# Optimization experiments

Hardware: AMD Instinct MI355X
Metric: run time of the kernel (lower is better)

## Reference

```python
import jax, jax.numpy as jnp
import numpy as np

LN_EPS = 1e-5

def layer_norm(x, w, b):
    m = jnp.mean(x, axis=-1, keepdims=True)
    v = jnp.mean((x - m) ** 2, axis=-1, keepdims=True)
    return (x - m) * jax.lax.rsqrt(v + LN_EPS) * w + b

def setup_inputs() -> dict:
    key = jax.random.key(0)
    ks = jax.random.split(key, 10)
    B, N, L = 32, 576, 100
    low, high = 1024, 1536
    inp = {
        "vit_feat": jax.random.normal(ks[0], (B, N, low), dtype=jnp.float32),
        "box_feat": jax.random.normal(ks[1], (B, L, high), dtype=jnp.float32),
        "lengths": jax.random.randint(ks[2], (B,), 0, L, dtype=jnp.int64),
        # query projector: LayerNorm(low) + Linear(low, low)
        "q_ln_w": jnp.ones((low,), jnp.float32),
        "q_ln_b": jnp.zeros((low,), jnp.float32),
        "q_w": jax.random.normal(ks[3], (low, low), dtype=jnp.float32) * 0.02,
        "q_b": jnp.zeros((low,), jnp.float32),
        # key projector: LayerNorm(high) + Linear(high, low)
        "k_ln_w": jnp.ones((high,), jnp.float32),
        "k_ln_b": jnp.zeros((high,), jnp.float32),
        "k_w": jax.random.normal(ks[4], (high, low), dtype=jnp.float32) * 0.02,
        "k_b": jnp.zeros((low,), jnp.float32),
        # value projector: LayerNorm(high) + Linear(high, low)
        "v_ln_w": jnp.ones((high,), jnp.float32),
        "v_ln_b": jnp.zeros((high,), jnp.float32),
        "v_w": jax.random.normal(ks[5], (high, low), dtype=jnp.float32) * 0.02,
        "v_b": jnp.zeros((low,), jnp.float32),
    }
    return inp

def reference(vit_feat, box_feat, lengths,
              q_ln_w, q_ln_b, q_w, q_b,
              k_ln_w, k_ln_b, k_w, k_b,
              v_ln_w, v_ln_b, v_w, v_b):
    B, L = box_feat.shape[0], box_feat.shape[1]
    # padding mask, same as the original per-row copy loop
    mask = jnp.arange(L)[None, :] < lengths[:, None]          # [B, L] bool
    q = layer_norm(vit_feat, q_ln_w, q_ln_b) @ q_w + q_b      # [B, N, low]
    k = layer_norm(box_feat, k_ln_w, k_ln_b) @ k_w + k_b      # [B, L, low]
    v = layer_norm(box_feat, v_ln_w, v_ln_b) @ v_w + v_b      # [B, L, low]
    scale = 1.0 / jnp.sqrt(jnp.asarray(k.shape[-1], q.dtype))
    att = jnp.einsum('bnd,bld->bnl', q, k * scale)            # [B, N, L]
    att = jnp.where(mask[:, None, :], att, -jnp.inf)
    att = jnp.nan_to_num(att)  # -inf -> finite min, matching torch nan_to_num
    att = jax.nn.softmax(att, axis=-1)
    out = jnp.einsum('bnl,bld->bnd', att, v)                  # [B, N, low]
    return vit_feat + out
```

## Files before the change

kernel.cpp:

```cpp
#include <hip/hip_runtime.h>
#include <stdint.h>

typedef __attribute__((ext_vector_type(8))) short short8;
typedef __attribute__((ext_vector_type(4))) float f32x4;

#define NEG_FLT_MAX (-3.402823466e38f)

__device__ __forceinline__ unsigned short f2bf(float f) {
  uint32_t u = __float_as_uint(f);
  uint32_t r = (u + 0x7fffu + ((u >> 16) & 1u)) >> 16;
  return (unsigned short)r;
}

__device__ __forceinline__ float bf2f(unsigned short u) {
  return __uint_as_float(((uint32_t)u) << 16);
}

__device__ __forceinline__ void gload16(const void* g, void* l) {
  __builtin_amdgcn_global_load_lds(
      (const __attribute__((address_space(1))) uint32_t*)g,
      (__attribute__((address_space(3))) uint32_t*)l, 16, 0, 0);
}

__global__ void tpv_kernel(const float* __restrict__ src, unsigned short* __restrict__ dst) {
  __shared__ float tile[32][33];
  const int c0 = blockIdx.x * 32;
  const int r0 = blockIdx.y * 32;
  const int tx = threadIdx.x, ty = threadIdx.y;
#pragma unroll
  for (int i = ty; i < 32; i += 8)
    tile[i][tx] = src[(size_t)(r0 + i) * 1024 + (c0 + tx)];
  __syncthreads();
#pragma unroll
  for (int i = ty; i < 32; i += 8)
    dst[(size_t)(c0 + i) * 1536 + (r0 + tx)] = f2bf(tile[tx][i]);
}

__global__ __launch_bounds__(256) void wconv_kernel(
    const float* __restrict__ qw, const float* __restrict__ kw,
    unsigned short* __restrict__ qwb, unsigned short* __restrict__ kwb, float scale) {
  const int idx = blockIdx.x * 256 + threadIdx.x;
  const int QG = 1024 * 1024 / 4;
  if (idx < QG) {
    float4 v = ((const float4*)qw)[idx];
    ushort4 o;
    o.x = f2bf(v.x); o.y = f2bf(v.y); o.z = f2bf(v.z); o.w = f2bf(v.w);
    ((ushort4*)qwb)[idx] = o;
  } else {
    const int j = idx - QG;
    float4 v = ((const float4*)kw)[j];
    ushort4 o;
    o.x = f2bf(v.x * scale); o.y = f2bf(v.y * scale);
    o.z = f2bf(v.z * scale); o.w = f2bf(v.w * scale);
    ((ushort4*)kwb)[j] = o;
  }
}

__global__ __launch_bounds__(256) void wvec_kernel(
    const float* __restrict__ qw, const float* __restrict__ kw,
    const float* __restrict__ qb, const float* __restrict__ kb, float scale,
    float* __restrict__ bias3, float* __restrict__ w4, float* __restrict__ c4) {
  const int wv = threadIdx.x >> 6, l = threadIdx.x & 63;
  const int idx = blockIdx.x;
  float s = 0.f;
  if (idx < 256) {
    const int i = idx * 4 + wv;
    const float* row = qw + (size_t)i * 1024;
#pragma unroll
    for (int s0 = 0; s0 < 1024; s0 += 256) {
      float4 a = *(const float4*)(row + s0 + l * 4);
      float4 b = *(const float4*)(kb + s0 + l * 4);
      s += a.x * b.x + a.y * b.y + a.z * b.z + a.w * b.w;
    }
#pragma unroll
    for (int off = 32; off; off >>= 1) s += __shfl_xor(s, off);
    if (l == 0) bias3[i] = s * scale;
  } else if (idx < 640) {
    const int j = (idx - 256) * 4 + wv;
    const float* row = kw + (size_t)j * 1024;
#pragma unroll
    for (int s0 = 0; s0 < 1024; s0 += 256) {
      float4 a = *(const float4*)(row + s0 + l * 4);
      float4 b = *(const float4*)(qb + s0 + l * 4);
      s += a.x * b.x + a.y * b.y + a.z * b.z + a.w * b.w;
    }
#pragma unroll
    for (int off = 32; off; off >>= 1) s += __shfl_xor(s, off);
    if (l == 0) w4[j] = s * scale;
  } else if (wv == 0) {
#pragma unroll
    for (int s0 = 0; s0 < 1024; s0 += 256) {
      float4 a = *(const float4*)(qb + s0 + l * 4);
      float4 b = *(const float4*)(kb + s0 + l * 4);
      s += a.x * b.x + a.y * b.y + a.z * b.z + a.w * b.w;
    }
#pragma unroll
    for (int off = 32; off; off >>= 1) s += __shfl_xor(s, off);
    if (l == 0) *c4 = s * scale;
  }
}

__device__ __forceinline__ void block_reduce2(float& s, float& ss, float* red) {
#pragma unroll
  for (int off = 32; off > 0; off >>= 1) {
    s += __shfl_xor(s, off);
    ss += __shfl_xor(ss, off);
  }
  const int wave = threadIdx.x >> 6;
  const int lane = threadIdx.x & 63;
  if (lane == 0) { red[wave * 2] = s; red[wave * 2 + 1] = ss; }
  __syncthreads();
  if (threadIdx.x == 0) {
    float a = 0.f, b = 0.f;
    for (int i = 0; i < 4; i++) { a += red[i * 2]; b += red[i * 2 + 1]; }
    red[0] = a; red[1] = b;
  }
  __syncthreads();
  s = red[0]; ss = red[1];
}

__global__ __launch_bounds__(256) void ln_vit_kernel(
    const float* __restrict__ x, const float* __restrict__ w,
    const float* __restrict__ b, unsigned short* __restrict__ out) {
  __shared__ float red[8];
  const int row = blockIdx.x;
  const int t = threadIdx.x;
  const float4 v = ((const float4*)(x + (size_t)row * 1024))[t];
  float s = v.x + v.y + v.z + v.w;
  float ss = v.x * v.x + v.y * v.y + v.z * v.z + v.w * v.w;
  block_reduce2(s, ss, red);
  const float m = s * (1.f / 1024.f);
  const float var = ss * (1.f / 1024.f) - m * m;
  const float rstd = rsqrtf(var + 1e-5f);
  const float4 w4 = ((const float4*)w)[t];
  const float4 b4 = ((const float4*)b)[t];
  ushort4 o;
  o.x = f2bf((v.x - m) * rstd * w4.x + b4.x);
  o.y = f2bf((v.y - m) * rstd * w4.y + b4.y);
  o.z = f2bf((v.z - m) * rstd * w4.z + b4.z);
  o.w = f2bf((v.w - m) * rstd * w4.w + b4.w);
  ((ushort4*)(out + (size_t)row * 1024))[t] = o;
}

__global__ __launch_bounds__(256) void ln_box_kernel(
    const float* __restrict__ x,
    const float* __restrict__ kw, const float* __restrict__ kb,
    const float* __restrict__ vw, const float* __restrict__ vb,
    unsigned short* __restrict__ kn, unsigned short* __restrict__ vn) {
  __shared__ float red[8];
  const int row = blockIdx.x;
  const int t = threadIdx.x;
  const float4* xr = (const float4*)(x + (size_t)row * 1536);
  const float4 a = xr[t];
  float4 c = make_float4(0.f, 0.f, 0.f, 0.f);
  if (t < 128) c = xr[256 + t];
  float s = a.x + a.y + a.z + a.w + c.x + c.y + c.z + c.w;
  float ss = a.x * a.x + a.y * a.y + a.z * a.z + a.w * a.w +
             c.x * c.x + c.y * c.y + c.z * c.z + c.w * c.w;
  block_reduce2(s, ss, red);
  const float m = s * (1.f / 1536.f);
  const float var = ss * (1.f / 1536.f) - m * m;
  const float rstd = rsqrtf(var + 1e-5f);
  {
    const float4 w4 = ((const float4*)kw)[t];
    const float4 b4 = ((const float4*)kb)[t];
    ushort4 o;
    o.x = f2bf((a.x - m) * rstd * w4.x + b4.x);
    o.y = f2bf((a.y - m) * rstd * w4.y + b4.y);
    o.z = f2bf((a.z - m) * rstd * w4.z + b4.z);
    o.w = f2bf((a.w - m) * rstd * w4.w + b4.w);
    ((ushort4*)(kn + (size_t)row * 1536))[t] = o;
    const float4 w4v = ((const float4*)vw)[t];
    const float4 b4v = ((const float4*)vb)[t];
    o.x = f2bf((a.x - m) * rstd * w4v.x + b4v.x);
    o.y = f2bf((a.y - m) * rstd * w4v.y + b4v.y);
    o.z = f2bf((a.z - m) * rstd * w4v.z + b4v.z);
    o.w = f2bf((a.w - m) * rstd * w4v.w + b4v.w);
    ((ushort4*)(vn + (size_t)row * 1536))[t] = o;
  }
  if (t < 128) {
    const int t2 = 256 + t;
    const float4 w4 = ((const float4*)kw)[t2];
    const float4 b4 = ((const float4*)kb)[t2];
    ushort4 o;
    o.x = f2bf((c.x - m) * rstd * w4.x + b4.x);
    o.y = f2bf((c.y - m) * rstd * w4.y + b4.y);
    o.z = f2bf((c.z - m) * rstd * w4.z + b4.z);
    o.w = f2bf((c.w - m) * rstd * w4.w + b4.w);
    ((ushort4*)(kn + (size_t)row * 1536))[t2] = o;
    const float4 w4v = ((const float4*)vw)[t2];
    const float4 b4v = ((const float4*)vb)[t2];
    o.x = f2bf((c.x - m) * rstd * w4v.x + b4v.x);
    o.y = f2bf((c.y - m) * rstd * w4v.y + b4v.y);
    o.z = f2bf((c.z - m) * rstd * w4v.z + b4v.z);
    o.w = f2bf((c.w - m) * rstd * w4v.w + b4v.w);
    ((ushort4*)(vn + (size_t)row * 1536))[t2] = o;
  }
}

__global__ __launch_bounds__(256) void qbk_kernel(
    const unsigned short* __restrict__ kn, const float* __restrict__ w4,
    const float* __restrict__ c4, float* __restrict__ qbk) {
  const int wv = threadIdx.x >> 6, l = threadIdx.x & 63;
  const int row = blockIdx.x * 4 + wv;
  const unsigned short* r = kn + (size_t)row * 1536;
  float s = 0.f;
#pragma unroll
  for (int s0 = 0; s0 < 1536; s0 += 512) {
    short8 v = *(const short8*)(r + s0 + l * 8);
    const float* wp = w4 + s0 + l * 8;
    float4 w0 = *(const float4*)wp;
    float4 w1 = *(const float4*)(wp + 4);
    s += bf2f((unsigned short)v[0]) * w0.x + bf2f((unsigned short)v[1]) * w0.y +
         bf2f((unsigned short)v[2]) * w0.z + bf2f((unsigned short)v[3]) * w0.w +
         bf2f((unsigned short)v[4]) * w1.x + bf2f((unsigned short)v[5]) * w1.y +
         bf2f((unsigned short)v[6]) * w1.z + bf2f((unsigned short)v[7]) * w1.w;
  }
#pragma unroll
  for (int off = 32; off; off >>= 1) s += __shfl_xor(s, off);
  if (l == 0) qbk[row] = s + *c4;
}

__device__ __forceinline__ void gemm_core64(
    const unsigned short* __restrict__ A, int lda, int rowmaxA, int tm0,
    const unsigned short* __restrict__ Bt, int ldb, int rowmaxB, int tn0,
    int K, unsigned short* As, unsigned short* Bs, f32x4 acc[4][4]) {
  const int tid = threadIdx.x;
  const int w = tid >> 6, l = tid & 63;
  const int wr = w >> 1, wc = w & 1;
  const int srow = (w << 4) + (l >> 2);
  const int scol = (l & 3) << 3;
  int ra0 = tm0 + srow;      if (ra0 > rowmaxA) ra0 = rowmaxA;
  int ra1 = tm0 + srow + 64; if (ra1 > rowmaxA) ra1 = rowmaxA;
  int rb0 = tn0 + srow;      if (rb0 > rowmaxB) rb0 = rowmaxB;
  int rb1 = tn0 + srow + 64; if (rb1 > rowmaxB) rb1 = rowmaxB;
  const unsigned short* pa0 = A + (size_t)ra0 * lda + scol;
  const unsigned short* pa1 = A + (size_t)ra1 * lda + scol;
  const unsigned short* pb0 = Bt + (size_t)rb0 * ldb + scol;
  const unsigned short* pb1 = Bt + (size_t)rb1 * ldb + scol;
  unsigned short* la0 = As + (w << 4) * 32;
  unsigned short* la1 = As + ((w << 4) + 64) * 32;
  unsigned short* lb0 = Bs + (w << 4) * 32;
  unsigned short* lb1 = Bs + ((w << 4) + 64) * 32;
  const int foff = ((l & 15) << 5) + ((l >> 4) << 3);
  const unsigned short* fa = As + (wr << 6) * 32 + foff;
  const unsigned short* fb = Bs + (wc << 6) * 32 + foff;
#pragma unroll
  for (int i = 0; i < 4; i++)
#pragma unroll
    for (int j = 0; j < 4; j++) acc[i][j] = (f32x4)0.0f;
  for (int k0 = 0; k0 < K; k0 += 64) {
    gload16(pa0 + k0, la0);
    gload16(pa1 + k0, la1);
    gload16(pb0 + k0, lb0);
    gload16(pb1 + k0, lb1);
    gload16(pa0 + k0 + 32, la0 + 4096);
    gload16(pa1 + k0 + 32, la1 + 4096);
    gload16(pb0 + k0 + 32, lb0 + 4096);
    gload16(pb1 + k0 + 32, lb1 + 4096);
    __syncthreads();
    {
      short8 a[4], b[4];
#pragma unroll
      for (int i = 0; i < 4; i++) a[i] = *(const short8*)(fa + i * 512);
#pragma unroll
      for (int j = 0; j < 4; j++) b[j] = *(const short8*)(fb + j * 512);
#pragma unroll
      for (int i = 0; i < 4; i++)
#pragma unroll
        for (int j = 0; j < 4; j++)
          acc[i][j] = __builtin_amdgcn_mfma_f32_16x16x32_bf16(a[i], b[j], acc[i][j], 0, 0, 0);
    }
    {
      short8 a[4], b[4];
#pragma unroll
      for (int i = 0; i < 4; i++) a[i] = *(const short8*)(fa + 4096 + i * 512);
#pragma unroll
      for (int j = 0; j < 4; j++) b[j] = *(const short8*)(fb + 4096 + j * 512);
#pragma unroll
      for (int i = 0; i < 4; i++)
#pragma unroll
        for (int j = 0; j < 4; j++)
          acc[i][j] = __builtin_amdgcn_mfma_f32_16x16x32_bf16(a[i], b[j], acc[i][j], 0, 0, 0);
    }
    __syncthreads();
  }
}

__global__ __launch_bounds__(256) void gemm_w3_kernel(
    const unsigned short* __restrict__ qwb, const unsigned short* __restrict__ kwb,
    unsigned short* __restrict__ W3) {
  __shared__ unsigned short As[128 * 64];
  __shared__ unsigned short Bs[128 * 64];
  const int tm0 = blockIdx.x * 128, tn0 = blockIdx.y * 128;
  f32x4 acc[4][4];
  gemm_core64(qwb, 1024, 1023, tm0, kwb, 1024, 1535, tn0, 1024, As, Bs, acc);
  const int tid = threadIdx.x;
  const int w = tid >> 6, l = tid & 63;
  const int wr = w >> 1, wc = w & 1;
#pragma unroll
  for (int i = 0; i < 4; i++) {
    const int row0 = tm0 + wr * 64 + i * 16 + (l >> 4) * 4;
#pragma unroll
    for (int j = 0; j < 4; j++) {
      const int col = tn0 + wc * 64 + j * 16 + (l & 15);
#pragma unroll
      for (int r = 0; r < 4; r++)
        W3[(size_t)(row0 + r) * 1536 + col] = f2bf(acc[i][j][r]);
    }
  }
}

__global__ __launch_bounds__(256) void gemm_kv_kernel(
    const unsigned short* __restrict__ kn, const unsigned short* __restrict__ vn,
    const unsigned short* __restrict__ W3, const unsigned short* __restrict__ vwt,
    const float* __restrict__ bias3, const float* __restrict__ vb,
    unsigned short* __restrict__ kq, unsigned short* __restrict__ vT) {
  __shared__ unsigned short As[128 * 64];
  __shared__ unsigned short Bs[128 * 64];
  const int z = blockIdx.z;
  const unsigned short* A = z ? vn : kn;
  const unsigned short* Bt = z ? vwt : W3;
  const float* bias = z ? vb : bias3;
  const int M = 3200, N = 1024, K = 1536;
  const int tm0 = blockIdx.x * 128, tn0 = blockIdx.y * 128;
  f32x4 acc[4][4];
  gemm_core64(A, K, M - 1, tm0, Bt, K, N - 1, tn0, K, As, Bs, acc);
  const int tid = threadIdx.x;
  const int w = tid >> 6, l = tid & 63;
  const int wr = w >> 1, wc = w & 1;
#pragma unroll
  for (int i = 0; i < 4; i++) {
    const int row0 = tm0 + wr * 64 + i * 16 + (l >> 4) * 4;
#pragma unroll
    for (int j = 0; j < 4; j++) {
      const int col = tn0 + wc * 64 + j * 16 + (l & 15);
      const float bv = bias[col];
#pragma unroll
      for (int r = 0; r < 4; r++) {
        const int row = row0 + r;
        const float val = acc[i][j][r] + bv;
        if (!z) {
          kq[(size_t)row * N + col] = f2bf(val);
        } else {
          const int bb = row / 100;
          const int ll = row - bb * 100;
          vT[((size_t)bb * N + col) * 128 + ll] = f2bf(val);
        }
      }
    }
  }
}

__global__ __launch_bounds__(256) void attfused_kernel(
    const unsigned short* __restrict__ qn, const unsigned short* __restrict__ kq,
    const unsigned short* __restrict__ vT, const float* __restrict__ qbk,
    const int* __restrict__ lengths, const float* __restrict__ vit,
    float* __restrict__ out) {
  __shared__ __align__(16) char smem[53248];
  unsigned short* As = (unsigned short*)smem;
  unsigned short* Bs = (unsigned short*)(smem + 8192);
  float* Smat = (float*)smem;
  float* invr = (float*)(smem + 34816);
  float* qb_l = (float*)(smem + 35072);
  unsigned short* P = (unsigned short*)(smem + 36864);

  const int b = blockIdx.y;
  const int tm0 = blockIdx.x * 64;
  const int t = threadIdx.x;
  const int w = t >> 6, l = t & 63;
  if (t < 128) qb_l[t] = (t < 100) ? qbk[b * 100 + t] : 0.f;

  const unsigned short* A = qn + (size_t)b * 576 * 1024;
  const unsigned short* B = kq + (size_t)b * 100 * 1024;
  const int sr = t >> 2;
  const int sc8 = (t & 3) << 3;
  const unsigned short* pa = A + (size_t)(tm0 + sr) * 1024 + sc8;
  const unsigned short* pb0 = B + (size_t)sr * 1024 + sc8;
  int rb1 = 64 + sr; if (rb1 > 99) rb1 = 99;
  const unsigned short* pb1 = B + (size_t)rb1 * 1024 + sc8;
  unsigned short* la = As + (w << 9);
  unsigned short* lb0 = Bs + (w << 9);
  unsigned short* lb1 = Bs + 2048 + (w << 9);
  const int foff = ((l & 15) << 5) + ((l >> 4) << 3);
  const unsigned short* fa = As + foff;
  const unsigned short* fb = Bs + (w << 5) * 32 + foff;

  f32x4 acc[4][2];
#pragma unroll
  for (int i = 0; i < 4; i++) { acc[i][0] = (f32x4)0.0f; acc[i][1] = (f32x4)0.0f; }

  for (int k0 = 0; k0 < 1024; k0 += 64) {
    gload16(pa + k0, la);
    gload16(pb0 + k0, lb0);
    gload16(pb1 + k0, lb1);
    gload16(pa + k0 + 32, la + 2048);
    gload16(pb0 + k0 + 32, lb0 + 4096);
    gload16(pb1 + k0 + 32, lb1 + 4096);
    __syncthreads();
    {
      short8 a[4], bf[2];
#pragma unroll
      for (int i = 0; i < 4; i++) a[i] = *(const short8*)(fa + i * 512);
#pragma unroll
      for (int j = 0; j < 2; j++) bf[j] = *(const short8*)(fb + j * 512);
#pragma unroll
      for (int i = 0; i < 4; i++)
#pragma unroll
        for (int j = 0; j < 2; j++)
          acc[i][j] = __builtin_amdgcn_mfma_f32_16x16x32_bf16(a[i], bf[j], acc[i][j], 0, 0, 0);
    }
    {
      short8 a[4], bf[2];
#pragma unroll
      for (int i = 0; i < 4; i++) a[i] = *(const short8*)(fa + 2048 + i * 512);
#pragma unroll
      for (int j = 0; j < 2; j++) bf[j] = *(const short8*)(fb + 4096 + j * 512);
#pragma unroll
      for (int i = 0; i < 4; i++)
#pragma unroll
        for (int j = 0; j < 2; j++)
          acc[i][j] = __builtin_amdgcn_mfma_f32_16x16x32_bf16(a[i], bf[j], acc[i][j], 0, 0, 0);
    }
    __syncthreads();
  }

#pragma unroll
  for (int i = 0; i < 4; i++) {
    const int r0 = i * 16 + (l >> 4) * 4;
#pragma unroll
    for (int j = 0; j < 2; j++) {
      const int c = (w << 5) + j * 16 + (l & 15);
      const float qb = qb_l[c];
#pragma unroll
      for (int rr = 0; rr < 4; rr++) Smat[c * 68 + r0 + rr] = acc[i][j][rr] + qb;
    }
  }
  __syncthreads();

  const int r = t >> 2, g = t & 3;
  const int len = lengths[b];
  float mx = NEG_FLT_MAX;
#pragma unroll
  for (int i = 0; i < 25; i++) {
    const int ll = g * 25 + i;
    const float v = (ll < len) ? Smat[ll * 68 + r] : NEG_FLT_MAX;
    mx = fmaxf(mx, v);
  }
  mx = fmaxf(mx, __shfl_xor(mx, 1));
  mx = fmaxf(mx, __shfl_xor(mx, 2));
  float sum = 0.f;
#pragma unroll
  for (int i = 0; i < 25; i++) {
    const int ll = g * 25 + i;
    const float v = (ll < len) ? Smat[ll * 68 + r] : NEG_FLT_MAX;
    const float e = __expf(v - mx);
    Smat[ll * 68 + r] = e;
    sum += e;
  }
  sum += __shfl_xor(sum, 1);
  sum += __shfl_xor(sum, 2);
  if (g == 0) invr[r] = 1.f / sum;
  __syncthreads();

  {
    const float inv = invr[r];
    ushort4* prow = (ushort4*)(P + r * 128);
#pragma unroll
    for (int j = 0; j < 8; j++) {
      const int c0 = g * 32 + j * 4;
      ushort4 o;
      o.x = (c0 + 0 < 100) ? f2bf(Smat[(c0 + 0) * 68 + r] * inv) : (unsigned short)0;
      o.y = (c0 + 1 < 100) ? f2bf(Smat[(c0 + 1) * 68 + r] * inv) : (unsigned short)0;
      o.z = (c0 + 2 < 100) ? f2bf(Smat[(c0 + 2) * 68 + r] * inv) : (unsigned short)0;
      o.w = (c0 + 3 < 100) ? f2bf(Smat[(c0 + 3) * 68 + r] * inv) : (unsigned short)0;
      prow[g * 8 + j] = o;
    }
  }
  __syncthreads();

  const unsigned short* vTb = vT + (size_t)b * 131072;
  const float* vitb = vit + ((size_t)b * 576 + tm0) * 1024;
  float* outb = out + ((size_t)b * 576 + tm0) * 1024;
  for (int nt = 0; nt < 8; ++nt) {
    {
      const unsigned short* src = vTb + (size_t)nt * 16384 + ((t >> 4) * 128) + ((t & 15) * 8);
#pragma unroll
      for (int i = 0; i < 8; i++)
        gload16(src + i * 2048, smem + i * 4096 + w * 1024);
    }
    __syncthreads();
    f32x4 acc2[4][2];
#pragma unroll
    for (int i = 0; i < 4; i++) { acc2[i][0] = (f32x4)0.0f; acc2[i][1] = (f32x4)0.0f; }
#pragma unroll
    for (int ks = 0; ks < 4; ks++) {
      short8 av[4], bv[2];
#pragma unroll
      for (int i = 0; i < 4; i++)
        av[i] = *(const short8*)(smem + 36864 + (i * 16 + (l & 15)) * 256 + ks * 64 + ((l >> 4) << 4));
#pragma unroll
      for (int j = 0; j < 2; j++)
        bv[j] = *(const short8*)(smem + (w * 32 + j * 16 + (l & 15)) * 256 + ks * 64 + ((l >> 4) << 4));
#pragma unroll
      for (int i = 0; i < 4; i++)
#pragma unroll
        for (int j = 0; j < 2; j++)
          acc2[i][j] = __builtin_amdgcn_mfma_f32_16x16x32_bf16(av[i], bv[j], acc2[i][j], 0, 0, 0);
    }
    __syncthreads();
    {
      float* E = (float*)smem;
#pragma unroll
      for (int i = 0; i < 4; i++) {
        const int row0 = i * 16 + (l >> 4) * 4;
#pragma unroll
        for (int j = 0; j < 2; j++) {
          const int col = w * 32 + j * 16 + (l & 15);
#pragma unroll
          for (int rr = 0; rr < 4; rr++) E[(row0 + rr) * 128 + col] = acc2[i][j][rr];
        }
      }
    }
    __syncthreads();
    {
#pragma unroll
      for (int m = 0; m < 8; m++) {
        const int row = m * 8 + (t >> 5);
        const int colb = (t & 31) * 4;
        float4 e = *(const float4*)(smem + row * 512 + colb * 4);
        const size_t gidx = (size_t)row * 1024 + nt * 128 + colb;
        float4 vv = *(const float4*)(vitb + gidx);
        e.x += vv.x; e.y += vv.y; e.z += vv.z; e.w += vv.w;
        *(float4*)(outb + gidx) = e;
      }
    }
    __syncthreads();
  }
}

extern "C" void kernel_launch(void* const* d_in, const int* in_sizes, int n_in,
                              void* d_out, int out_size, void* d_ws, size_t ws_size,
                              hipStream_t stream) {
  const float* vit = (const float*)d_in[0];
  const float* box = (const float*)d_in[1];
  const int* lengths = (const int*)d_in[2];
  const float* q_ln_w = (const float*)d_in[3];
  const float* q_ln_b = (const float*)d_in[4];
  const float* q_w = (const float*)d_in[5];
  const float* q_b = (const float*)d_in[6];
  const float* k_ln_w = (const float*)d_in[7];
  const float* k_ln_b = (const float*)d_in[8];
  const float* k_w = (const float*)d_in[9];
  const float* k_b = (const float*)d_in[10];
  const float* v_ln_w = (const float*)d_in[11];
  const float* v_ln_b = (const float*)d_in[12];
  const float* v_w = (const float*)d_in[13];
  const float* v_b = (const float*)d_in[14];
  float* out = (float*)d_out;
  char* ws = (char*)d_ws;

  unsigned short* kn    = (unsigned short*)(ws + 0);
  unsigned short* vn    = (unsigned short*)(ws + 9830400);
  unsigned short* v_wt  = (unsigned short*)(ws + 19660800);
  unsigned short* qwb   = (unsigned short*)(ws + 22806528);
  unsigned short* kwb   = (unsigned short*)(ws + 24903680);
  unsigned short* W3    = (unsigned short*)(ws + 28049408);
  float*          bias3 = (float*)(ws + 31195136);
  float*          w4    = (float*)(ws + 31199232);
  float*          c4    = (float*)(ws + 31207424);
  unsigned short* qn    = (unsigned short*)(ws + 0);
  float*          qbk   = (float*)(ws + 37748736);
  unsigned short* kq    = (unsigned short*)(ws + 37761536);
  unsigned short* vT    = (unsigned short*)(ws + 44315136);

  const float scale = 0.03125f;

  wconv_kernel<<<2560, 256, 0, stream>>>(q_w, k_w, qwb, kwb, scale);
  tpv_kernel<<<dim3(32, 48), dim3(32, 8), 0, stream>>>(v_w, v_wt);
  wvec_kernel<<<641, 256, 0, stream>>>(q_w, k_w, q_b, k_b, scale, bias3, w4, c4);

  ln_box_kernel<<<3200, 256, 0, stream>>>(box, k_ln_w, k_ln_b, v_ln_w, v_ln_b, kn, vn);

  gemm_w3_kernel<<<dim3(8, 12), 256, 0, stream>>>(qwb, kwb, W3);

  qbk_kernel<<<800, 256, 0, stream>>>(kn, w4, c4, qbk);

  gemm_kv_kernel<<<dim3(25, 8, 2), 256, 0, stream>>>(
      kn, vn, W3, v_wt, bias3, v_b, kq, vT);

  ln_vit_kernel<<<18432, 256, 0, stream>>>(vit, q_ln_w, q_ln_b, qn);

  attfused_kernel<<<dim3(9, 32), 256, 0, stream>>>(
      qn, kq, vT, qbk, lengths, vit, out);

  (void)in_sizes; (void)n_in; (void)out_size; (void)ws_size;
}
```

Measured before the change: 178.4 us.

## Halve attention row tile to 32 and XOR-swizzle LDS for P, V and epilogue

```diff
diff --git a/kernel.cpp b/kernel.cpp
--- a/kernel.cpp
+++ b/kernel.cpp
@@ -357,124 +357,115 @@
     const unsigned short* __restrict__ vT, const float* __restrict__ qbk,
     const int* __restrict__ lengths, const float* __restrict__ vit,
     float* __restrict__ out) {
-  __shared__ __align__(16) char smem[53248];
-  unsigned short* As = (unsigned short*)smem;
-  unsigned short* Bs = (unsigned short*)(smem + 8192);
+  __shared__ __align__(16) char smem[62208];
   float* Smat = (float*)smem;
-  float* invr = (float*)(smem + 34816);
-  float* qb_l = (float*)(smem + 35072);
-  unsigned short* P = (unsigned short*)(smem + 36864);
+  float* invr = (float*)(smem + 28672);
+  float* qb_l = (float*)(smem + 28800);
+  const int PB = 20480, BV = 29440;
 
   const int b = blockIdx.y;
-  const int tm0 = blockIdx.x * 64;
+  const int tm0 = blockIdx.x * 32;
   const int t = threadIdx.x;
   const int w = t >> 6, l = t & 63;
+  const int lo = l & 15, hi = l >> 4;
   if (t < 128) qb_l[t] = (t < 100) ? qbk[b * 100 + t] : 0.f;
 
   const unsigned short* A = qn + (size_t)b * 576 * 1024;
   const unsigned short* B = kq + (size_t)b * 100 * 1024;
-  const int sr = t >> 2;
-  const int sc8 = (t & 3) << 3;
-  const unsigned short* pa = A + (size_t)(tm0 + sr) * 1024 + sc8;
-  const unsigned short* pb0 = B + (size_t)sr * 1024 + sc8;
-  int rb1 = 64 + sr; if (rb1 > 99) rb1 = 99;
-  const unsigned short* pb1 = B + (size_t)rb1 * 1024 + sc8;
-  unsigned short* la = As + (w << 9);
-  unsigned short* lb0 = Bs + (w << 9);
-  unsigned short* lb1 = Bs + 2048 + (w << 9);
-  const int foff = ((l & 15) << 5) + ((l >> 4) << 3);
-  const unsigned short* fa = As + foff;
-  const unsigned short* fb = Bs + (w << 5) * 32 + foff;
-
-  f32x4 acc[4][2];
-#pragma unroll
-  for (int i = 0; i < 4; i++) { acc[i][0] = (f32x4)0.0f; acc[i][1] = (f32x4)0.0f; }
+  const int ar = (t & 127) >> 2, ah = t >> 7, ac = (t & 3) << 3;
+  const unsigned short* paA = A + (size_t)(tm0 + ar) * 1024 + ah * 32 + ac;
+  const unsigned short* pbB[4];
+#pragma unroll
+  for (int i = 0; i < 4; i++) {
+    int rb = (i & 1) * 64 + (t >> 2); if (rb > 99) rb = 99;
+    pbB[i] = B + (size_t)rb * 1024 + (i >> 1) * 32 + ((t & 3) << 3);
+  }
+  const int cw = w << 5;
+
+  f32x4 acc[2][2];
+#pragma unroll
+  for (int i = 0; i < 2; i++) { acc[i][0] = (f32x4)0.0f; acc[i][1] = (f32x4)0.0f; }
 
   for (int k0 = 0; k0 < 1024; k0 += 64) {
-    gload16(pa + k0, la);
-    gload16(pb0 + k0, lb0);
-    gload16(pb1 + k0, lb1);
-    gload16(pa + k0 + 32, la + 2048);
-    gload16(pb0 + k0 + 32, lb0 + 4096);
-    gload16(pb1 + k0 + 32, lb1 + 4096);
-    __syncthreads();
-    {
-      short8 a[4], bf[2];
-#pragma unroll
-      for (int i = 0; i < 4; i++) a[i] = *(const short8*)(fa + i * 512);
-#pragma unroll
-      for (int j = 0; j < 2; j++) bf[j] = *(const short8*)(fb + j * 512);
-#pragma unroll
-      for (int i = 0; i < 4; i++)
+    gload16(paA + k0, smem + w * 1024);
+#pragma unroll
+    for (int i = 0; i < 4; i++)
+      gload16(pbB[i] + k0, smem + 4096 + i * 4096 + w * 1024);
+    __syncthreads();
+#pragma unroll
+    for (int half = 0; half < 2; half++) {
+      short8 a[2], bb[2];
+#pragma unroll
+      for (int i = 0; i < 2; i++)
+        a[i] = *(const short8*)(smem + half * 2048 + (i * 16 + lo) * 64 + hi * 16);
+#pragma unroll
+      for (int j = 0; j < 2; j++)
+        bb[j] = *(const short8*)(smem + 4096 + half * 8192 + (cw + j * 16 + lo) * 64 + hi * 16);
+#pragma unroll
+      for (int i = 0; i < 2; i++)
 #pragma unroll
         for (int j = 0; j < 2; j++)
-          acc[i][j] = __builtin_amdgcn_mfma_f32_16x16x32_bf16(a[i], bf[j], acc[i][j], 0, 0, 0);
-    }
-    {
-      short8 a[4], bf[2];
-#pragma unroll
-      for (int i = 0; i < 4; i++) a[i] = *(const short8*)(fa + 2048 + i * 512);
-#pragma unroll
-      for (int j = 0; j < 2; j++) bf[j] = *(const short8*)(fb + 4096 + j * 512);
-#pragma unroll
-      for (int i = 0; i < 4; i++)
-#pragma unroll
-        for (int j = 0; j < 2; j++)
-          acc[i][j] = __builtin_amdgcn_mfma_f32_16x16x32_bf16(a[i], bf[j], acc[i][j], 0, 0, 0);
-    }
-    __syncthreads();
-  }
-
-#pragma unroll
-  for (int i = 0; i < 4; i++) {
-    const int r0 = i * 16 + (l >> 4) * 4;
+          acc[i][j] = __builtin_amdgcn_mfma_f32_16x16x32_bf16(a[i], bb[j], acc[i][j], 0, 0, 0);
+    }
+    __syncthreads();
+  }
+
+#pragma unroll
+  for (int i = 0; i < 2; i++) {
+    const int r0 = i * 16 + hi * 4;
 #pragma unroll
     for (int j = 0; j < 2; j++) {
-      const int c = (w << 5) + j * 16 + (l & 15);
+      const int c = cw + j * 16 + lo;
       const float qb = qb_l[c];
 #pragma unroll
-      for (int rr = 0; rr < 4; rr++) Smat[c * 68 + r0 + rr] = acc[i][j][rr] + qb;
+      for (int rr = 0; rr < 4; rr++) Smat[c * 36 + r0 + rr] = acc[i][j][rr] + qb;
     }
   }
   __syncthreads();
 
-  const int r = t >> 2, g = t & 3;
+  const int r = t >> 3, g = t & 7;
   const int len = lengths[b];
   float mx = NEG_FLT_MAX;
 #pragma unroll
-  for (int i = 0; i < 25; i++) {
-    const int ll = g * 25 + i;
-    const float v = (ll < len) ? Smat[ll * 68 + r] : NEG_FLT_MAX;
-    mx = fmaxf(mx, v);
+  for (int i = 0; i < 13; i++) {
+    const int ll = g * 13 + i;
+    if (ll < 100) {
+      const float v = (ll < len) ? Smat[ll * 36 + r] : NEG_FLT_MAX;
+      mx = fmaxf(mx, v);
+    }
   }
   mx = fmaxf(mx, __shfl_xor(mx, 1));
   mx = fmaxf(mx, __shfl_xor(mx, 2));
+  mx = fmaxf(mx, __shfl_xor(mx, 4));
   float sum = 0.f;
 #pragma unroll
-  for (int i = 0; i < 25; i++) {
-    const int ll = g * 25 + i;
-    const float v = (ll < len) ? Smat[ll * 68 + r] : NEG_FLT_MAX;
-    const float e = __expf(v - mx);
-    Smat[ll * 68 + r] = e;
-    sum += e;
+  for (int i = 0; i < 13; i++) {
+    const int ll = g * 13 + i;
+    if (ll < 100) {
+      const float v = (ll < len) ? Smat[ll * 36 + r] : NEG_FLT_MAX;
+      const float e = __expf(v - mx);
+      Smat[ll * 36 + r] = e;
+      sum += e;
+    }
   }
   sum += __shfl_xor(sum, 1);
   sum += __shfl_xor(sum, 2);
+  sum += __shfl_xor(sum, 4);
   if (g == 0) invr[r] = 1.f / sum;
   __syncthreads();
 
   {
     const float inv = invr[r];
-    ushort4* prow = (ushort4*)(P + r * 128);
-#pragma unroll
-    for (int j = 0; j < 8; j++) {
-      const int c0 = g * 32 + j * 4;
+#pragma unroll
+    for (int jj = 0; jj < 4; jj++) {
+      const int c0 = g * 16 + jj * 4;
       ushort4 o;
-      o.x = (c0 + 0 < 100) ? f2bf(Smat[(c0 + 0) * 68 + r] * inv) : (unsigned short)0;
-      o.y = (c0 + 1 < 100) ? f2bf(Smat[(c0 + 1) * 68 + r] * inv) : (unsigned short)0;
-      o.z = (c0 + 2 < 100) ? f2bf(Smat[(c0 + 2) * 68 + r] * inv) : (unsigned short)0;
-      o.w = (c0 + 3 < 100) ? f2bf(Smat[(c0 + 3) * 68 + r] * inv) : (unsigned short)0;
-      prow[g * 8 + j] = o;
+      o.x = (c0 + 0 < 100) ? f2bf(Smat[(c0 + 0) * 36 + r] * inv) : (unsigned short)0;
+      o.y = (c0 + 1 < 100) ? f2bf(Smat[(c0 + 1) * 36 + r] * inv) : (unsigned short)0;
+      o.z = (c0 + 2 < 100) ? f2bf(Smat[(c0 + 2) * 36 + r] * inv) : (unsigned short)0;
+      o.w = (c0 + 3 < 100) ? f2bf(Smat[(c0 + 3) * 36 + r] * inv) : (unsigned short)0;
+      const int phys = (r * 256 + g * 32 + jj * 8) ^ ((r & 7) << 4);
+      *(ushort4*)(smem + PB + phys) = o;
     }
   }
   __syncthreads();
@@ -482,58 +473,58 @@
   const unsigned short* vTb = vT + (size_t)b * 131072;
   const float* vitb = vit + ((size_t)b * 576 + tm0) * 1024;
   float* outb = out + ((size_t)b * 576 + tm0) * 1024;
+  const int sBcol = ((t & 15) ^ ((t >> 4) & 7)) << 3;
   for (int nt = 0; nt < 8; ++nt) {
-    {
-      const unsigned short* src = vTb + (size_t)nt * 16384 + ((t >> 4) * 128) + ((t & 15) * 8);
-#pragma unroll
-      for (int i = 0; i < 8; i++)
-        gload16(src + i * 2048, smem + i * 4096 + w * 1024);
-    }
-    __syncthreads();
-    f32x4 acc2[4][2];
-#pragma unroll
-    for (int i = 0; i < 4; i++) { acc2[i][0] = (f32x4)0.0f; acc2[i][1] = (f32x4)0.0f; }
+#pragma unroll
+    for (int i = 0; i < 8; i++) {
+      const int vrow = nt * 128 + i * 16 + (t >> 4);
+      gload16(vTb + (size_t)vrow * 128 + sBcol, smem + BV + i * 4096 + w * 1024);
+    }
+    __syncthreads();
+    f32x4 acc2[2][2];
+#pragma unroll
+    for (int i = 0; i < 2; i++) { acc2[i][0] = (f32x4)0.0f; acc2[i][1] = (f32x4)0.0f; }
 #pragma unroll
     for (int ks = 0; ks < 4; ks++) {
-      short8 av[4], bv[2];
-#pragma unroll
-      for (int i = 0; i < 4; i++)
-        av[i] = *(const short8*)(smem + 36864 + (i * 16 + (l & 15)) * 256 + ks * 64 + ((l >> 4) << 4));
-#pragma unroll
-      for (int j = 0; j < 2; j++)
-        bv[j] = *(const short8*)(smem + (w * 32 + j * 16 + (l & 15)) * 256 + ks * 64 + ((l >> 4) << 4));
-#pragma unroll
-      for (int i = 0; i < 4; i++)
+      short8 av[2], bv[2];
+#pragma unroll
+      for (int i = 0; i < 2; i++) {
+        const int m = i * 16 + lo;
+        av[i] = *(const short8*)(smem + PB + ((m * 256 + ks * 64 + hi * 16) ^ ((m & 7) << 4)));
+      }
+#pragma unroll
+      for (int j = 0; j < 2; j++) {
+        const int n = cw + j * 16 + lo;
+        bv[j] = *(const short8*)(smem + BV + ((n * 256 + ks * 64 + hi * 16) ^ ((n & 7) << 4)));
+      }
+#pragma unroll
+      for (int i = 0; i < 2; i++)
 #pragma unroll
         for (int j = 0; j < 2; j++)
           acc2[i][j] = __builtin_amdgcn_mfma_f32_16x16x32_bf16(av[i], bv[j], acc2[i][j], 0, 0, 0);
     }
-    __syncthreads();
-    {
-      float* E = (float*)smem;
-#pragma unroll
-      for (int i = 0; i < 4; i++) {
-        const int row0 = i * 16 + (l >> 4) * 4;
-#pragma unroll
-        for (int j = 0; j < 2; j++) {
-          const int col = w * 32 + j * 16 + (l & 15);
-#pragma unroll
-          for (int rr = 0; rr < 4; rr++) E[(row0 + rr) * 128 + col] = acc2[i][j][rr];
+#pragma unroll
+    for (int i = 0; i < 2; i++) {
+#pragma unroll
+      for (int j = 0; j < 2; j++) {
+        const int col = cw + j * 16 + lo;
+#pragma unroll
+        for (int rr = 0; rr < 4; rr++) {
+          const int row = i * 16 + hi * 4 + rr;
+          *(float*)(smem + ((row * 512 + col * 4) ^ ((row & 7) << 4))) = acc2[i][j][rr];
         }
       }
     }
     __syncthreads();
-    {
-#pragma unroll
-      for (int m = 0; m < 8; m++) {
-        const int row = m * 8 + (t >> 5);
-        const int colb = (t & 31) * 4;
-        float4 e = *(const float4*)(smem + row * 512 + colb * 4);
-        const size_t gidx = (size_t)row * 1024 + nt * 128 + colb;
-        float4 vv = *(const float4*)(vitb + gidx);
-        e.x += vv.x; e.y += vv.y; e.z += vv.z; e.w += vv.w;
-        *(float4*)(outb + gidx) = e;
-      }
+#pragma unroll
+    for (int m = 0; m < 4; m++) {
+      const int row = m * 8 + (t >> 5);
+      const int colb = (t & 31) * 4;
+      float4 e = *(const float4*)(smem + ((row * 512 + colb * 4) ^ ((row & 7) << 4)));
+      const size_t gidx = (size_t)row * 1024 + nt * 128 + colb;
+      float4 vv = *(const float4*)(vitb + gidx);
+      e.x += vv.x; e.y += vv.y; e.z += vv.z; e.w += vv.w;
+      *(float4*)(outb + gidx) = e;
     }
     __syncthreads();
   }
@@ -591,7 +582,7 @@
 
   ln_vit_kernel<<<18432, 256, 0, stream>>>(vit, q_ln_w, q_ln_b, qn);
 
-  attfused_kernel<<<dim3(9, 32), 256, 0, stream>>>(
+  attfused_kernel<<<dim3(18, 32), 256, 0, stream>>>(
       qn, kq, vT, qbk, lengths, vit, out);
 
   (void)in_sizes; (void)n_in; (void)out_size; (void)ws_size;
```

New measurement: 180.2 us. Within noise of the previous version (+1.0%).
